# Optimization experiments

Measured on AMD Instinct MI355X. Metric: run time of the kernel, lower is better.

Reference implementation:

```python
import jax, jax.numpy as jnp
import numpy as np

N = 32768      # tokens
E = 2048       # embedding_dim
V = 256        # vq_dim
K = 256        # codebook size (levels=[256] -> single level, log2 K = 8)
HID = 1024     # condition MLP hidden dim
LOG2K = 8      # log2_num_embeddings
N_MID = 4      # condition_layer - 2 middle blocks
BN_EPS = 1e-5


def _normalize(x):
    return x / (jnp.linalg.norm(x, axis=-1, keepdims=True) + 1e-6)


def _bn(x, g, b):
    # BatchNorm1d, training-mode batch statistics over the codebook rows
    m = x.mean(0)
    v = x.var(0)
    return g * (x - m) * jax.lax.rsqrt(v + BN_EPS) + b


def _codebook(w0, b0, g0, be0, wm, bm, gm, bem, wL, bL):
    # get_bvectors(8, 256): binary expansion of 0..255, width 8 (no pad needed)
    ints = jnp.arange(K)
    bits = ((ints[:, None] >> jnp.arange(LOG2K - 1, -1, -1)[None, :]) & 1).astype(jnp.float32)
    x = jax.nn.relu(_bn(bits @ w0 + b0, g0, be0))
    for i in range(N_MID):
        x = jax.nn.relu(_bn(x @ wm[i] + bm[i], gm[i], bem[i]))
    return x @ wL + bL  # [K, V]


def setup_inputs() -> dict:
    key = jax.random.key(0)
    ks = jax.random.split(key, 8)
    def lin(k, fan_in, shape):
        return (jax.random.normal(k, shape, jnp.float32) / np.sqrt(fan_in)).astype(jnp.float32)
    return {
        "h_in": jax.random.normal(ks[0], (N, E), jnp.float32),
        "temp": jnp.array([0.3], jnp.float32),
        "proj_w": lin(ks[1], E, (E, V)), "proj_b": jnp.zeros((V,), jnp.float32),
        "pinv_w": lin(ks[2], V, (V, E)), "pinv_b": jnp.zeros((E,), jnp.float32),
        "w0": lin(ks[3], LOG2K, (LOG2K, HID)), "b0": jnp.zeros((HID,), jnp.float32),
        "g0": jnp.ones((HID,), jnp.float32), "be0": jnp.zeros((HID,), jnp.float32),
        "wm": lin(ks[4], HID, (N_MID, HID, HID)), "bm": jnp.zeros((N_MID, HID), jnp.float32),
        "gm": jnp.ones((N_MID, HID), jnp.float32), "bem": jnp.zeros((N_MID, HID), jnp.float32),
        "wL": lin(ks[5], HID, (HID, V)), "bL": jnp.zeros((V,), jnp.float32),
    }


def reference(h_in, temp, proj_w, proj_b, pinv_w, pinv_b,
              w0, b0, g0, be0, wm, bm, gm, bem, wL, bL):
    # forward(h_in, mode='eval', temperature=1, level=256); levels=[256] -> idx_all=1
    h = _normalize(h_in @ proj_w + proj_b)                          # proj + sphere normalize, [N, V]
    embed = _normalize(_codebook(w0, b0, g0, be0, wm, bm, gm, bem, wL, bL))  # [K, V]

    # attention(): distance logits with temperature-scaled detached term
    sim = h @ embed.T                                               # [N, K]
    alpha = 1.0 / temp ** 2
    distances = -2.0 * (alpha - 1.0) * jax.lax.stop_gradient(sim) - 2.0 * sim
    A = jax.nn.softmax(-distances, axis=1)                          # [N, K]

    k_code, k_p = jax.random.split(jax.random.key(42))
    code = jax.random.categorical(k_code, -distances, axis=-1)      # multinomial(A, 1), [N]
    onehot = jax.nn.one_hot(code, K, dtype=A.dtype)
    c = onehot * (1.0 - A) + (1.0 - onehot) * (-A)
    A2 = A + jax.lax.stop_gradient(c)                               # fwd value == onehot
    h_vq = h + A2 @ embed - jax.lax.stop_gradient(h)                # straight-through quantize
    vq_loss = jnp.linalg.norm(h_vq - h, axis=-1).mean()             # idx_all == 1

    # select = (0 < p) & (p < 1) since idx=0, idx_all=1
    p = jax.random.uniform(k_p, (h.shape[0],))
    select = (0.0 < p) & (p < 1.0)
    quantized = h_vq * select[:, None].astype(h_vq.dtype)
    probs = A * select[:, None].astype(A.dtype)
    vq_code = code * select.astype(code.dtype)

    quantized_inv = quantized @ pinv_w + pinv_b                     # [N, E]
    return quantized_inv, vq_code, quantized, probs, vq_loss
```

## Files before the change

### kernel.cpp

```cpp
#include <hip/hip_runtime.h>
#include <hip/hip_bf16.h>
#include <stdint.h>
#include <stddef.h>

#ifndef PARTITIONABLE
#define PARTITIONABLE 1
#endif

typedef __attribute__((ext_vector_type(8))) short short8;
typedef __attribute__((ext_vector_type(4))) short short4v;
typedef __attribute__((ext_vector_type(4))) float f32x4;

__host__ __device__ __forceinline__ uint32_t rotl32(uint32_t x, int d){ return (x<<d)|(x>>(32-d)); }

__host__ __device__ __forceinline__ void tf4(uint32_t&x0, uint32_t&x1, int r0,int r1,int r2,int r3){
  x0+=x1; x1=rotl32(x1,r0); x1^=x0;
  x0+=x1; x1=rotl32(x1,r1); x1^=x0;
  x0+=x1; x1=rotl32(x1,r2); x1^=x0;
  x0+=x1; x1=rotl32(x1,r3); x1^=x0;
}
__host__ __device__ __forceinline__ void threefry2x32(uint32_t k0,uint32_t k1,uint32_t x0,uint32_t x1,
                                                      uint32_t&y0,uint32_t&y1){
  uint32_t ks2 = k0^k1^0x1BD11BDAu;
  x0+=k0; x1+=k1;
  tf4(x0,x1,13,15,26,6);  x0+=k1;  x1+=ks2+1u;
  tf4(x0,x1,17,29,16,24); x0+=ks2; x1+=k0+2u;
  tf4(x0,x1,13,15,26,6);  x0+=k0;  x1+=k1+3u;
  tf4(x0,x1,17,29,16,24); x0+=k1;  x1+=ks2+4u;
  tf4(x0,x1,13,15,26,6);  x0+=ks2; x1+=k0+5u;
  y0=x0; y1=x1;
}

__device__ __forceinline__ uint32_t random_bits32(uint32_t k0,uint32_t k1,uint32_t idx, uint32_t half){
#if PARTITIONABLE
  uint32_t y0,y1; threefry2x32(k0,k1, 0u, idx, y0,y1);
  (void)half;
  return y0 ^ y1;
#else
  uint32_t y0,y1;
  if (idx < half) { threefry2x32(k0,k1, idx, idx+half, y0,y1); return y0; }
  else            { threefry2x32(k0,k1, idx-half, idx, y0,y1); return y1; }
#endif
}

__device__ __forceinline__ unsigned short bf16_rne(float x){
  unsigned u = __float_as_uint(x);
  unsigned r = (u + 0x7FFFu + ((u>>16)&1u)) >> 16;
  return (unsigned short)r;
}
__device__ __forceinline__ float bf16_tof(unsigned short h){
  return __uint_as_float(((unsigned)h)<<16);
}
__device__ __forceinline__ void split8(const float* src, short8& hi, short8& lo){
  #pragma unroll
  for (int e=0;e<8;e++){
    unsigned short h = bf16_rne(src[e]);
    hi[e] = (short)h;
    lo[e] = (short)bf16_rne(src[e] - bf16_tof(h));
  }
}
__device__ __forceinline__ void split4(const float* src, short4v& hi, short4v& lo){
  #pragma unroll
  for (int e=0;e<4;e++){
    unsigned short h = bf16_rne(src[e]);
    hi[e] = (short)h;
    lo[e] = (short)bf16_rne(src[e] - bf16_tof(h));
  }
}

__device__ __forceinline__ void gll16(const void* g, void* l){
  __builtin_amdgcn_global_load_lds(
      (const __attribute__((address_space(1))) unsigned int*)g,
      (__attribute__((address_space(3))) unsigned int*)l, 16, 0, 0);
}

__device__ __forceinline__ void mk1_gemm(const float* __restrict__ A, int lda,
                                         const unsigned short* __restrict__ packB,
                                         int K, char* smem, f32x4 (&acc)[2][4]){
  const int tid=threadIdx.x, lane=tid&63, wv=tid>>6;
  const int wr=wv>>2, wc=wv&3;
  const int arow=tid>>3, aseg=tid&7, swA=(arow>>1)&3;
  unsigned short* Ahi=(unsigned short*)smem;
  unsigned short* Alo=(unsigned short*)(smem+4096);
  unsigned short* Bhi=(unsigned short*)(smem+8192);
  unsigned short* Blo=(unsigned short*)(smem+24576);
  const int NT=K/32;
  const int sA = arow*32 + ((aseg>>1)^swA)*8 + (aseg&1)*4;
  const int seg = wv*2;

  float4 av = *(const float4*)(A + (size_t)arow*lda + aseg*4);
  for(int t=0;t<NT;t++){
    __syncthreads();
    {
      float af[4]={av.x,av.y,av.z,av.w}; short4v vh,vl; split4(af,vh,vl);
      *(short4v*)&Ahi[sA]=vh; *(short4v*)&Alo[sA]=vl;
      const unsigned short* src = packB + (size_t)t*16384;
      #pragma unroll
      for(int q=0;q<2;q++){
        gll16(src + (seg+q)*512 + lane*8,        (char*)Bhi + (seg+q)*1024);
        gll16(src + 8192 + (seg+q)*512 + lane*8, (char*)Blo + (seg+q)*1024);
      }
      if (t+1<NT) av = *(const float4*)(A + (size_t)arow*lda + (t+1)*32 + aseg*4);
    }
    __syncthreads();
    short8 ah[2],al[2],bh[4],bl[4];
    const int kg=lane>>4;
    #pragma unroll
    for(int i=0;i<2;i++){
      const int r = wr*32 + i*16 + (lane&15);
      const int offA = r*32 + ((kg ^ ((r>>1)&3))*8);
      ah[i]=*(const short8*)&Ahi[offA]; al[i]=*(const short8*)&Alo[offA];
    }
    #pragma unroll
    for(int j=0;j<4;j++){
      const int c = wc*64 + j*16 + (lane&15);
      const int offB = c*32 + ((kg ^ ((c>>1)&3))*8);
      bh[j]=*(const short8*)&Bhi[offB]; bl[j]=*(const short8*)&Blo[offB];
    }
    #pragma unroll
    for(int i=0;i<2;i++)
      #pragma unroll
      for(int j=0;j<4;j++){
        acc[i][j]=__builtin_amdgcn_mfma_f32_16x16x32_bf16(ah[i],bh[j],acc[i][j],0,0,0);
        acc[i][j]=__builtin_amdgcn_mfma_f32_16x16x32_bf16(ah[i],bl[j],acc[i][j],0,0,0);
        acc[i][j]=__builtin_amdgcn_mfma_f32_16x16x32_bf16(al[i],bh[j],acc[i][j],0,0,0);
      }
  }
}

__global__ __launch_bounds__(256) void pack_w_kernel(const float* __restrict__ W,
                                                     unsigned short* __restrict__ pack){
  const int t = blockIdx.x>>2, s = blockIdx.x&3, c = threadIdx.x;
  const int g = s ^ ((c>>1)&3);
  const float* p = W + (size_t)(t*32 + g*8)*256 + c;
  float bf[8];
  #pragma unroll
  for(int e=0;e<8;e++) bf[e]=p[(size_t)e*256];
  short8 h,l; split8(bf,h,l);
  unsigned short* dst = pack + (size_t)t*16384 + c*32 + s*8;
  *(short8*)dst = h;
  *(short8*)(dst+8192) = l;
}

__device__ __forceinline__ void bn_block_t(float (&acc)[4], int col0,
                                           const float* __restrict__ gma,
                                           const float* __restrict__ bta,
                                           float* __restrict__ Yt,
                                           float* Zs, float* red, float* mcol, float* vcol){
  const int r = threadIdx.x;
  #pragma unroll
  for (int j=0;j<4;j++) Zs[r*5+j] = acc[j];
  __syncthreads();
  if (r < 16){
    const int rl = r & 3, j = r >> 2;
    float s = 0.f;
    for (int rr=rl; rr<256; rr+=4) s += Zs[rr*5+j];
    red[rl*4+j] = s;
  }
  __syncthreads();
  if (r < 4)
    mcol[r] = (red[0*4+r]+red[1*4+r]+red[2*4+r]+red[3*4+r]) * (1.0f/256.0f);
  __syncthreads();
  if (r < 16){
    const int rl = r & 3, j = r >> 2;
    const float m = mcol[j];
    float s2 = 0.f;
    for (int rr=rl; rr<256; rr+=4){ float d = Zs[rr*5+j]-m; s2 += d*d; }
    red[rl*4+j] = s2;
  }
  __syncthreads();
  if (r < 4)
    vcol[r] = (red[0*4+r]+red[1*4+r]+red[2*4+r]+red[3*4+r]) * (1.0f/256.0f);
  __syncthreads();
  #pragma unroll
  for (int j=0;j<4;j++){
    const int c = col0 + j;
    const float scale = gma[c] * rsqrtf(vcol[j] + 1e-5f);
    const float sh = bta[c];
    const float v = (acc[j]-mcol[j])*scale + sh;
    Yt[(size_t)c*256 + r] = v > 0.f ? v : 0.f;
  }
}

__global__ __launch_bounds__(256) void mlp_layer2_kernel(
    const float* __restrict__ Xt, const float* __restrict__ W,
    const float* __restrict__ bias,
    const float* __restrict__ gma, const float* __restrict__ bta,
    float* __restrict__ Yt){
  __shared__ float Ws[1024*2];
  __shared__ float Zs[256*3];
  __shared__ float red[8], mcol[2], vcol[2];
  const int r = threadIdx.x;
  const int col0 = blockIdx.x*2;
  #pragma unroll
  for (int q=0;q<4;q++){
    const int k = q*256 + r;
    const float2 wv = *(const float2*)&W[(size_t)k*1024 + col0];
    *(float2*)&Ws[k*2] = wv;
  }
  __syncthreads();
  float acc0=0.f, acc1=0.f;
  #pragma unroll 16
  for (int k=0;k<1024;k++){
    const float a = Xt[(size_t)k*256 + r];
    acc0 += a*Ws[k*2];
    acc1 += a*Ws[k*2+1];
  }
  acc0 += bias[col0]; acc1 += bias[col0+1];
  Zs[r*3+0]=acc0; Zs[r*3+1]=acc1;
  __syncthreads();
  if (r < 8){
    const int rl = r & 3, j = r >> 2;
    float s=0.f;
    for (int rr=rl; rr<256; rr+=4) s += Zs[rr*3+j];
    red[rl*2+j] = s;
  }
  __syncthreads();
  if (r < 2) mcol[r] = (red[0*2+r]+red[1*2+r]+red[2*2+r]+red[3*2+r])*(1.0f/256.0f);
  __syncthreads();
  if (r < 8){
    const int rl = r & 3, j = r >> 2;
    const float m = mcol[j];
    float s2=0.f;
    for (int rr=rl; rr<256; rr+=4){ float d = Zs[rr*3+j]-m; s2 += d*d; }
    red[rl*2+j] = s2;
  }
  __syncthreads();
  if (r < 2) vcol[r] = (red[0*2+r]+red[1*2+r]+red[2*2+r]+red[3*2+r])*(1.0f/256.0f);
  __syncthreads();
  {
    const float s0 = gma[col0] * rsqrtf(vcol[0] + 1e-5f);
    const float v0 = (acc0-mcol[0])*s0 + bta[col0];
    Yt[(size_t)col0*256 + r] = v0 > 0.f ? v0 : 0.f;
    const float s1 = gma[col0+1] * rsqrtf(vcol[1] + 1e-5f);
    const float v1 = (acc1-mcol[1])*s1 + bta[col0+1];
    Yt[(size_t)(col0+1)*256 + r] = v1 > 0.f ? v1 : 0.f;
  }
}

__global__ __launch_bounds__(256) void mlp_l0t_kernel(
    const float* __restrict__ w0, const float* __restrict__ b0,
    const float* __restrict__ g0, const float* __restrict__ be0,
    float* __restrict__ Yt){
  __shared__ float Zs[256*5];
  __shared__ float red[16], mcol[4], vcol[4];
  const int i = threadIdx.x;
  const int col0 = blockIdx.x*4;
  float acc[4];
  #pragma unroll
  for (int j=0;j<4;j++) acc[j] = b0[col0+j];
  #pragma unroll
  for (int jj=0;jj<8;jj++){
    if ((i >> (7-jj)) & 1){
      #pragma unroll
      for (int j=0;j<4;j++) acc[j] += w0[jj*1024 + col0 + j];
    }
  }
  bn_block_t(acc, col0, g0, be0, Yt, Zs, red, mcol, vcol);
}

__global__ __launch_bounds__(256) void mlp_tail_kernel(
    const float* __restrict__ Xt,
    const float* __restrict__ wL, const float* __restrict__ bL,
    const float* __restrict__ pinv_w, const float* __restrict__ pinv_b,
    float* __restrict__ embed, unsigned short* __restrict__ packE,
    float* __restrict__ Epp){
  __shared__ float xrow[1024];
  __shared__ float erow[256];
  __shared__ float wsum[4];
  const int n = blockIdx.x, t = threadIdx.x;
  #pragma unroll
  for (int q=0;q<4;q++) xrow[q*256+t] = Xt[(size_t)(q*256+t)*256 + n];
  __syncthreads();
  float acc = 0.f;
  #pragma unroll 16
  for (int k=0;k<1024;k++) acc += xrow[k] * wL[(size_t)k*256 + t];
  acc += bL[t];
  const int lane = t & 63, wv = t >> 6;
  float v = acc*acc;
  #pragma unroll
  for (int o=32;o;o>>=1) v += __shfl_xor(v,o);
  if (lane==0) wsum[wv]=v;
  __syncthreads();
  const float total = wsum[0]+wsum[1]+wsum[2]+wsum[3];
  const float inv = 1.0f/(sqrtf(total)+1e-6f);
  const float y = acc*inv;
  embed[(size_t)n*256+t] = y;
  erow[t] = y;
  {
    unsigned short h = bf16_rne(y);
    unsigned short l = bf16_rne(y - bf16_tof(h));
    const int tt=t>>5, kk=t&31, g=kk>>3, e=kk&7, s=g^((n>>1)&3);
    unsigned short* d = packE + (size_t)tt*16384 + n*32 + s*8 + e;
    d[0] = h; d[8192] = l;
  }
  __syncthreads();
  float a8[8] = {0.f,0.f,0.f,0.f,0.f,0.f,0.f,0.f};
  #pragma unroll 8
  for (int k=0;k<256;k++){
    const float ev = erow[k];
    const float4 w0v = *(const float4*)&pinv_w[(size_t)k*2048 + t*8];
    const float4 w1v = *(const float4*)&pinv_w[(size_t)k*2048 + t*8 + 4];
    a8[0] += ev*w0v.x; a8[1] += ev*w0v.y; a8[2] += ev*w0v.z; a8[3] += ev*w0v.w;
    a8[4] += ev*w1v.x; a8[5] += ev*w1v.y; a8[6] += ev*w1v.z; a8[7] += ev*w1v.w;
  }
  #pragma unroll
  for (int j=0;j<8;j++) a8[j] += pinv_b[t*8+j];
  float4* dst = (float4*)(Epp + (size_t)n*2048 + t*8);
  dst[0] = (float4){a8[0],a8[1],a8[2],a8[3]};
  dst[1] = (float4){a8[4],a8[5],a8[6],a8[7]};
}

__global__ __launch_bounds__(512) void proj_norm_kernel(
    const float* __restrict__ A, const unsigned short* __restrict__ packW,
    const float* __restrict__ bias, float* __restrict__ Hn, int K){
  __shared__ char smem[40960];
  f32x4 acc[2][4];
  #pragma unroll
  for (int i=0;i<2;i++)
    #pragma unroll
    for (int j=0;j<4;j++) acc[i][j] = (f32x4){0.f,0.f,0.f,0.f};
  const int bm = blockIdx.x * 64;
  mk1_gemm(A + (size_t)bm*K, K, packW, K, smem, acc);
  __syncthreads();

  const int tid = threadIdx.x, lane = tid&63, wv = tid>>6;
  const int wr = wv>>2, wc = wv&3;
  float* ns = (float*)smem;
  #pragma unroll
  for (int j=0;j<4;j++){
    const int c = wc*64 + j*16 + (lane&15);
    const float bb = bias[c];
    #pragma unroll
    for (int i=0;i<2;i++)
      #pragma unroll
      for (int reg=0;reg<4;reg++) acc[i][j][reg] += bb;
  }
  #pragma unroll
  for (int i=0;i<2;i++)
    #pragma unroll
    for (int reg=0;reg<4;reg++){
      float p = acc[i][0][reg]*acc[i][0][reg] + acc[i][1][reg]*acc[i][1][reg]
              + acc[i][2][reg]*acc[i][2][reg] + acc[i][3][reg]*acc[i][3][reg];
      #pragma unroll
      for (int o=1;o<16;o<<=1) p += __shfl_xor(p, o);
      if ((lane&15)==0) ns[wc*64 + wr*32 + i*16 + (lane>>4)*4 + reg] = p;
    }
  __syncthreads();
  #pragma unroll
  for (int i=0;i<2;i++){
    const int rl = wr*32 + i*16 + (lane>>4)*4;
    #pragma unroll
    for (int reg=0;reg<4;reg++){
      const int r = rl + reg;
      const float tot = ns[0*64+r]+ns[1*64+r]+ns[2*64+r]+ns[3*64+r];
      const float inv = 1.0f/(sqrtf(tot)+1e-6f);
      const size_t grow = (size_t)(bm + r);
      #pragma unroll
      for (int j=0;j<4;j++){
        const int c = wc*64 + j*16 + (lane&15);
        Hn[grow*256 + c] = acc[i][j][reg]*inv;
      }
    }
  }
}

__global__ __launch_bounds__(512) void sim_sample_kernel(
    const float* __restrict__ Hn, const unsigned short* __restrict__ packE,
    const float* __restrict__ embed, const float* __restrict__ temp,
    float* __restrict__ probs, float* __restrict__ codef,
    float* __restrict__ quant, float* __restrict__ norms,
    const float* __restrict__ Epp, const float* __restrict__ pinv_b,
    float* __restrict__ q_inv,
    uint32_t kc0, uint32_t kc1, uint32_t kp0, uint32_t kp1){
  __shared__ char smem[40960];
  f32x4 acc[2][4];
  #pragma unroll
  for (int i=0;i<2;i++)
    #pragma unroll
    for (int j=0;j<4;j++) acc[i][j] = (f32x4){0.f,0.f,0.f,0.f};
  const int bm = blockIdx.x * 64;
  mk1_gemm(Hn + (size_t)bm*256, 256, packE, 256, smem, acc);
  __syncthreads();

  float* redf = (float*)smem;
  int*   redi = (int*)(smem+1024);
  float* smax = (float*)(smem+2048);
  float* ssum = (float*)(smem+2304);
  float* ssel = (float*)(smem+2560);
  int*  scode = (int*)(smem+2816);

  const int tid = threadIdx.x, lane = tid&63, wv = tid>>6;
  const int wr = wv>>2, wc = wv&3;
  const float tv = temp[0];
  const float alpha = 1.0f/(tv*tv);
  #pragma unroll
  for (int i=0;i<2;i++)
    #pragma unroll
    for (int j=0;j<4;j++)
      #pragma unroll
      for (int reg=0;reg<4;reg++){
        const float s = acc[i][j][reg];
        const float dist = -2.0f*(alpha-1.0f)*s - 2.0f*s;
        acc[i][j][reg] = -dist;
      }
  #pragma unroll
  for (int i=0;i<2;i++)
    #pragma unroll
    for (int reg=0;reg<4;reg++){
      float m = fmaxf(fmaxf(acc[i][0][reg], acc[i][1][reg]),
                      fmaxf(acc[i][2][reg], acc[i][3][reg]));
      #pragma unroll
      for (int o=1;o<16;o<<=1) m = fmaxf(m, __shfl_xor(m, o));
      if ((lane&15)==0) redf[wc*64 + wr*32 + i*16 + (lane>>4)*4 + reg] = m;
    }
  __syncthreads();
  if (tid < 64)
    smax[tid] = fmaxf(fmaxf(redf[0*64+tid], redf[1*64+tid]), fmaxf(redf[2*64+tid], redf[3*64+tid]));
  __syncthreads();
  #pragma unroll
  for (int i=0;i<2;i++)
    #pragma unroll
    for (int reg=0;reg<4;reg++){
      const int r = wr*32 + i*16 + (lane>>4)*4 + reg;
      const float m = smax[r];
      float p = expf(acc[i][0][reg]-m) + expf(acc[i][1][reg]-m)
              + expf(acc[i][2][reg]-m) + expf(acc[i][3][reg]-m);
      #pragma unroll
      for (int o=1;o<16;o<<=1) p += __shfl_xor(p, o);
      if ((lane&15)==0) redf[wc*64 + r] = p;
    }
  __syncthreads();
  if (tid < 64){
    ssum[tid] = redf[0*64+tid]+redf[1*64+tid]+redf[2*64+tid]+redf[3*64+tid];
    const uint32_t pb = random_bits32(kp0,kp1,(uint32_t)(bm+tid), 16384u);
    const float pf = __uint_as_float((pb>>9) | 0x3f800000u) - 1.0f;
    ssel[tid] = (pf > 0.0f) ? 1.0f : 0.0f;
  }
  __syncthreads();
  #pragma unroll
  for (int i=0;i<2;i++)
    #pragma unroll
    for (int reg=0;reg<4;reg++){
      const int r = wr*32 + i*16 + (lane>>4)*4 + reg;
      const uint32_t grow = (uint32_t)(bm + r);
      float zb = -1e38f; int ib = 0x7fffffff;
      #pragma unroll
      for (int j=0;j<4;j++){
        const int c = wc*64 + j*16 + (lane&15);
        const uint32_t bits = random_bits32(kc0,kc1, grow*256u + (uint32_t)c, 4194304u);
        const float f = __uint_as_float((bits>>9) | 0x3f800000u) - 1.0f;
        const float TINY = 1.17549435082228751e-38f;
        const float u = fmaxf(TINY, f + TINY);
        const float g = -logf(-logf(u));
        const float z = acc[i][j][reg] + g;
        if (z > zb || (z == zb && c < ib)){ zb = z; ib = c; }
      }
      #pragma unroll
      for (int o=1;o<16;o<<=1){
        const float zo = __shfl_xor(zb, o); const int io = __shfl_xor(ib, o);
        if (zo > zb || (zo == zb && io < ib)){ zb = zo; ib = io; }
      }
      if ((lane&15)==0){ redf[wc*64 + r] = zb; redi[wc*64 + r] = ib; }
    }
  __syncthreads();
  if (tid < 64){
    float zb = redf[0*64+tid]; int ib = redi[0*64+tid];
    #pragma unroll
    for (int w=1; w<4; w++)
      if (redf[w*64+tid] > zb || (redf[w*64+tid] == zb && redi[w*64+tid] < ib)){
        zb = redf[w*64+tid]; ib = redi[w*64+tid];
      }
    scode[tid] = ib;
  }
  __syncthreads();
  #pragma unroll
  for (int i=0;i<2;i++)
    #pragma unroll
    for (int reg=0;reg<4;reg++){
      const int r = wr*32 + i*16 + (lane>>4)*4 + reg;
      const size_t grow = (size_t)(bm + r);
      const float m = smax[r], sum = ssum[r], sel = ssel[r];
      const int code = scode[r];
      float p2 = 0.f;
      #pragma unroll
      for (int j=0;j<4;j++){
        const int c = wc*64 + j*16 + (lane&15);
        const float e = expf(acc[i][j][reg] - m);
        probs[grow*256 + c] = (e/sum) * sel;
        const float ev = embed[(size_t)code*256 + c];
        quant[grow*256 + c] = ev * sel;
        const float d = ev - Hn[grow*256 + c];
        p2 += d*d;
      }
      #pragma unroll
      for (int o=1;o<16;o<<=1) p2 += __shfl_xor(p2, o);
      if ((lane&15)==0) redf[wc*64 + r] = p2;
    }
  __syncthreads();
  if (tid < 64){
    norms[bm+tid] = sqrtf(redf[0*64+tid]+redf[1*64+tid]+redf[2*64+tid]+redf[3*64+tid]);
    codef[bm+tid] = (float)scode[tid] * ssel[tid];
  }
  #pragma unroll
  for (int rr=0; rr<8; rr++){
    const int r = wv*8 + rr;
    const int code = scode[r];
    const float sel = ssel[r];
    const float4* s4 = (const float4*)((sel != 0.0f) ? (Epp + (size_t)code*2048) : pinv_b);
    float4* dst = (float4*)(q_inv + (size_t)(bm + r)*2048);
    #pragma unroll
    for (int q=0;q<8;q++) dst[q*64 + lane] = s4[q*64 + lane];
  }
}

__global__ __launch_bounds__(256) void loss_kernel(const float* __restrict__ norms,
                                                   float* __restrict__ outp){
  const int t = threadIdx.x;
  float s = 0.f;
  for (int i=t;i<32768;i+=256) s += norms[i];
  #pragma unroll
  for (int o=32;o;o>>=1) s += __shfl_xor(s,o);
  __shared__ float wred[4];
  if ((t&63)==0) wred[t>>6]=s;
  __syncthreads();
  if (t==0) outp[0] = (wred[0]+wred[1]+wred[2]+wred[3]) * (1.0f/32768.0f);
}

extern "C" void kernel_launch(void* const* d_in, const int* in_sizes, int n_in,
                              void* d_out, int out_size, void* d_ws, size_t ws_size,
                              hipStream_t stream){
  const float* h_in  = (const float*)d_in[0];
  const float* temp  = (const float*)d_in[1];
  const float* proj_w= (const float*)d_in[2];
  const float* proj_b= (const float*)d_in[3];
  const float* pinv_w= (const float*)d_in[4];
  const float* pinv_b= (const float*)d_in[5];
  const float* w0 = (const float*)d_in[6];
  const float* b0 = (const float*)d_in[7];
  const float* g0 = (const float*)d_in[8];
  const float* be0= (const float*)d_in[9];
  const float* wm = (const float*)d_in[10];
  const float* bm = (const float*)d_in[11];
  const float* gm = (const float*)d_in[12];
  const float* bem= (const float*)d_in[13];
  const float* wL = (const float*)d_in[14];
  const float* bL = (const float*)d_in[15];

  float* out = (float*)d_out;
  float* q_inv  = out;
  float* o_code = out + 67108864;
  float* o_quant= out + 67141632;
  float* o_probs= out + 75530240;
  float* o_loss = out + 83918848;

  float* ws = (float*)d_ws;
  float* Hn     = ws + 0;
  float* XtA    = ws + 8388608;
  float* XtB    = ws + 8650752;
  float* embed  = ws + 8912896;
  float* norms  = ws + 8978432;
  float* Epp    = ws + 9076736;
  unsigned short* packW = (unsigned short*)(ws + 9601024);
  unsigned short* packE = (unsigned short*)(ws + 10125312);

  uint32_t kc0,kc1,kp0,kp1;
#if PARTITIONABLE
  threefry2x32(0u,42u, 0u,0u, kc0,kc1);
  threefry2x32(0u,42u, 0u,1u, kp0,kp1);
#else
  { uint32_t a0,b0w,a1,b1w;
    threefry2x32(0u,42u, 0u,2u, a0,b0w);
    threefry2x32(0u,42u, 1u,3u, a1,b1w);
    kc0=a0; kc1=a1; kp0=b0w; kp1=b1w; }
#endif

  pack_w_kernel<<<256,256,0,stream>>>(proj_w, packW);

  proj_norm_kernel<<<512,512,0,stream>>>(h_in, packW, proj_b, Hn, 2048);

  mlp_l0t_kernel<<<256,256,0,stream>>>(w0, b0, g0, be0, XtA);
  mlp_layer2_kernel<<<512,256,0,stream>>>(XtA, wm + 0*1048576, bm + 0*1024, gm + 0*1024, bem + 0*1024, XtB);
  mlp_layer2_kernel<<<512,256,0,stream>>>(XtB, wm + 1*1048576, bm + 1*1024, gm + 1*1024, bem + 1*1024, XtA);
  mlp_layer2_kernel<<<512,256,0,stream>>>(XtA, wm + 2*1048576, bm + 2*1024, gm + 2*1024, bem + 2*1024, XtB);
  mlp_layer2_kernel<<<512,256,0,stream>>>(XtB, wm + 3*1048576, bm + 3*1024, gm + 3*1024, bem + 3*1024, XtA);
  mlp_tail_kernel<<<256,256,0,stream>>>(XtA, wL, bL, pinv_w, pinv_b, embed, packE, Epp);

  sim_sample_kernel<<<512,512,0,stream>>>(Hn, packE, embed, temp,
                                          o_probs, o_code, o_quant, norms,
                                          Epp, pinv_b, q_inv,
                                          kc0,kc1,kp0,kp1);
  loss_kernel<<<1,256,0,stream>>>(norms, o_loss);
}
```

Baseline: 521.5 us.

## Fuse codebook MLP chain into one persistent kernel with grid barriers

Replaces the weight-pack kernel and the six separate codebook MLP kernels (first layer, four middle layers, tail) with one 256-block persistent kernel. The layers are separated by a software grid barrier built on atomic flags that are reset by a memset. Each block now handles four columns per middle layer instead of two, so only half as many blocks are needed. The aim is to remove launch overhead and inter-kernel gaps on the small serial MLP chain. The risks are deadlock if the 256 blocks are not all co-resident, and barrier spin cost.

```diff
diff --git a/kernel.cpp b/kernel.cpp
--- a/kernel.cpp
+++ b/kernel.cpp
@@ -128,18 +128,24 @@
   }
 }
 
-__global__ __launch_bounds__(256) void pack_w_kernel(const float* __restrict__ W,
-                                                     unsigned short* __restrict__ pack){
-  const int t = blockIdx.x>>2, s = blockIdx.x&3, c = threadIdx.x;
-  const int g = s ^ ((c>>1)&3);
-  const float* p = W + (size_t)(t*32 + g*8)*256 + c;
-  float bf[8];
-  #pragma unroll
-  for(int e=0;e<8;e++) bf[e]=p[(size_t)e*256];
-  short8 h,l; split8(bf,h,l);
-  unsigned short* dst = pack + (size_t)t*16384 + c*32 + s*8;
-  *(short8*)dst = h;
-  *(short8*)(dst+8192) = l;
+__device__ __forceinline__ void xbar(uint32_t gen, uint32_t* flags, uint32_t* release){
+  __syncthreads();
+  if (threadIdx.x == 0){
+    __threadfence();
+    __hip_atomic_store(&flags[blockIdx.x], gen, __ATOMIC_RELAXED, __HIP_MEMORY_SCOPE_AGENT);
+  }
+  if (blockIdx.x == 0){
+    while (__hip_atomic_load(&flags[threadIdx.x], __ATOMIC_RELAXED, __HIP_MEMORY_SCOPE_AGENT) < gen)
+      __builtin_amdgcn_s_sleep(16);
+    __syncthreads();
+    if (threadIdx.x == 0)
+      __hip_atomic_store(release, gen, __ATOMIC_RELAXED, __HIP_MEMORY_SCOPE_AGENT);
+  } else if (threadIdx.x == 0){
+    while (__hip_atomic_load(release, __ATOMIC_RELAXED, __HIP_MEMORY_SCOPE_AGENT) < gen)
+      __builtin_amdgcn_s_sleep(16);
+  }
+  __syncthreads();
+  __threadfence();
 }
 
 __device__ __forceinline__ void bn_block_t(float (&acc)[4], int col0,
@@ -182,31 +188,9 @@
   }
 }
 
-__global__ __launch_bounds__(256) void mlp_layer2_kernel(
-    const float* __restrict__ Xt, const float* __restrict__ W,
-    const float* __restrict__ bias,
-    const float* __restrict__ gma, const float* __restrict__ bta,
-    float* __restrict__ Yt){
-  __shared__ float Ws[1024*2];
-  __shared__ float Zs[256*3];
-  __shared__ float red[8], mcol[2], vcol[2];
-  const int r = threadIdx.x;
-  const int col0 = blockIdx.x*2;
-  #pragma unroll
-  for (int q=0;q<4;q++){
-    const int k = q*256 + r;
-    const float2 wv = *(const float2*)&W[(size_t)k*1024 + col0];
-    *(float2*)&Ws[k*2] = wv;
-  }
-  __syncthreads();
-  float acc0=0.f, acc1=0.f;
-  #pragma unroll 16
-  for (int k=0;k<1024;k++){
-    const float a = Xt[(size_t)k*256 + r];
-    acc0 += a*Ws[k*2];
-    acc1 += a*Ws[k*2+1];
-  }
-  acc0 += bias[col0]; acc1 += bias[col0+1];
+__device__ __forceinline__ void bn2(float acc0, float acc1, int col0,
+    const float* __restrict__ gma, const float* __restrict__ bta, float* __restrict__ Yt,
+    float* Zs, float* red, float* mcol, float* vcol, int r){
   Zs[r*3+0]=acc0; Zs[r*3+1]=acc1;
   __syncthreads();
   if (r < 8){
@@ -228,87 +212,146 @@
   __syncthreads();
   if (r < 2) vcol[r] = (red[0*2+r]+red[1*2+r]+red[2*2+r]+red[3*2+r])*(1.0f/256.0f);
   __syncthreads();
-  {
-    const float s0 = gma[col0] * rsqrtf(vcol[0] + 1e-5f);
-    const float v0 = (acc0-mcol[0])*s0 + bta[col0];
-    Yt[(size_t)col0*256 + r] = v0 > 0.f ? v0 : 0.f;
-    const float s1 = gma[col0+1] * rsqrtf(vcol[1] + 1e-5f);
-    const float v1 = (acc1-mcol[1])*s1 + bta[col0+1];
-    Yt[(size_t)(col0+1)*256 + r] = v1 > 0.f ? v1 : 0.f;
-  }
-}
-
-__global__ __launch_bounds__(256) void mlp_l0t_kernel(
+  const float s0 = gma[col0] * rsqrtf(vcol[0] + 1e-5f);
+  const float v0 = (acc0-mcol[0])*s0 + bta[col0];
+  Yt[(size_t)col0*256 + r] = v0 > 0.f ? v0 : 0.f;
+  const float s1 = gma[col0+1] * rsqrtf(vcol[1] + 1e-5f);
+  const float v1 = (acc1-mcol[1])*s1 + bta[col0+1];
+  Yt[(size_t)(col0+1)*256 + r] = v1 > 0.f ? v1 : 0.f;
+}
+
+__device__ void mid_layer(int b, int r, char* um,
+    const float* __restrict__ Xt, const float* __restrict__ W,
+    const float* __restrict__ bias,
+    const float* __restrict__ gma, const float* __restrict__ bta,
+    float* __restrict__ Yt){
+  float* Ws  = (float*)um;
+  float* Zs  = (float*)(um+16384);
+  float* red = (float*)(um+19456);
+  float* mcol= (float*)(um+19488);
+  float* vcol= (float*)(um+19496);
+  const int cA = b*2, cB = b*2 + 512;
+  #pragma unroll
+  for (int q=0;q<4;q++){
+    const int k = q*256 + r;
+    const float2 wa = *(const float2*)&W[(size_t)k*1024 + cA];
+    const float2 wb = *(const float2*)&W[(size_t)k*1024 + cB];
+    *(float4*)&Ws[k*4] = (float4){wa.x, wa.y, wb.x, wb.y};
+  }
+  __syncthreads();
+  float a0=0.f,a1=0.f,a2=0.f,a3=0.f;
+  #pragma unroll 16
+  for (int k=0;k<1024;k++){
+    const float a = Xt[(size_t)k*256 + r];
+    const float4 wv = *(const float4*)&Ws[k*4];
+    a0 += a*wv.x; a1 += a*wv.y; a2 += a*wv.z; a3 += a*wv.w;
+  }
+  a0 += bias[cA]; a1 += bias[cA+1]; a2 += bias[cB]; a3 += bias[cB+1];
+  bn2(a0, a1, cA, gma, bta, Yt, Zs, red, mcol, vcol, r);
+  __syncthreads();
+  bn2(a2, a3, cB, gma, bta, Yt, Zs, red, mcol, vcol, r);
+}
+
+__global__ __launch_bounds__(256) void uber_mlp_kernel(
+    const float* __restrict__ proj_w, unsigned short* __restrict__ packW,
     const float* __restrict__ w0, const float* __restrict__ b0,
     const float* __restrict__ g0, const float* __restrict__ be0,
-    float* __restrict__ Yt){
-  __shared__ float Zs[256*5];
-  __shared__ float red[16], mcol[4], vcol[4];
-  const int i = threadIdx.x;
-  const int col0 = blockIdx.x*4;
-  float acc[4];
-  #pragma unroll
-  for (int j=0;j<4;j++) acc[j] = b0[col0+j];
-  #pragma unroll
-  for (int jj=0;jj<8;jj++){
-    if ((i >> (7-jj)) & 1){
-      #pragma unroll
-      for (int j=0;j<4;j++) acc[j] += w0[jj*1024 + col0 + j];
-    }
-  }
-  bn_block_t(acc, col0, g0, be0, Yt, Zs, red, mcol, vcol);
-}
-
-__global__ __launch_bounds__(256) void mlp_tail_kernel(
-    const float* __restrict__ Xt,
+    const float* __restrict__ wm, const float* __restrict__ bm_a,
+    const float* __restrict__ gm, const float* __restrict__ bem,
     const float* __restrict__ wL, const float* __restrict__ bL,
     const float* __restrict__ pinv_w, const float* __restrict__ pinv_b,
+    float* __restrict__ XtA, float* __restrict__ XtB,
     float* __restrict__ embed, unsigned short* __restrict__ packE,
-    float* __restrict__ Epp){
-  __shared__ float xrow[1024];
-  __shared__ float erow[256];
-  __shared__ float wsum[4];
-  const int n = blockIdx.x, t = threadIdx.x;
-  #pragma unroll
-  for (int q=0;q<4;q++) xrow[q*256+t] = Xt[(size_t)(q*256+t)*256 + n];
-  __syncthreads();
-  float acc = 0.f;
-  #pragma unroll 16
-  for (int k=0;k<1024;k++) acc += xrow[k] * wL[(size_t)k*256 + t];
-  acc += bL[t];
-  const int lane = t & 63, wv = t >> 6;
-  float v = acc*acc;
-  #pragma unroll
-  for (int o=32;o;o>>=1) v += __shfl_xor(v,o);
-  if (lane==0) wsum[wv]=v;
-  __syncthreads();
-  const float total = wsum[0]+wsum[1]+wsum[2]+wsum[3];
-  const float inv = 1.0f/(sqrtf(total)+1e-6f);
-  const float y = acc*inv;
-  embed[(size_t)n*256+t] = y;
-  erow[t] = y;
+    float* __restrict__ Epp,
+    uint32_t* __restrict__ flags, uint32_t* __restrict__ release){
+  __shared__ char um[20608];
+  const int b = blockIdx.x, tid = threadIdx.x;
+
   {
-    unsigned short h = bf16_rne(y);
-    unsigned short l = bf16_rne(y - bf16_tof(h));
-    const int tt=t>>5, kk=t&31, g=kk>>3, e=kk&7, s=g^((n>>1)&3);
-    unsigned short* d = packE + (size_t)tt*16384 + n*32 + s*8 + e;
-    d[0] = h; d[8192] = l;
-  }
-  __syncthreads();
-  float a8[8] = {0.f,0.f,0.f,0.f,0.f,0.f,0.f,0.f};
-  #pragma unroll 8
-  for (int k=0;k<256;k++){
-    const float ev = erow[k];
-    const float4 w0v = *(const float4*)&pinv_w[(size_t)k*2048 + t*8];
-    const float4 w1v = *(const float4*)&pinv_w[(size_t)k*2048 + t*8 + 4];
-    a8[0] += ev*w0v.x; a8[1] += ev*w0v.y; a8[2] += ev*w0v.z; a8[3] += ev*w0v.w;
-    a8[4] += ev*w1v.x; a8[5] += ev*w1v.y; a8[6] += ev*w1v.z; a8[7] += ev*w1v.w;
-  }
-  #pragma unroll
-  for (int j=0;j<8;j++) a8[j] += pinv_b[t*8+j];
-  float4* dst = (float4*)(Epp + (size_t)n*2048 + t*8);
-  dst[0] = (float4){a8[0],a8[1],a8[2],a8[3]};
-  dst[1] = (float4){a8[4],a8[5],a8[6],a8[7]};
+    const int t = b>>2, s = b&3, c = tid;
+    const int g = s ^ ((c>>1)&3);
+    const float* p = proj_w + (size_t)(t*32 + g*8)*256 + c;
+    float bf[8];
+    #pragma unroll
+    for(int e=0;e<8;e++) bf[e]=p[(size_t)e*256];
+    short8 h,l; split8(bf,h,l);
+    unsigned short* dst = packW + (size_t)t*16384 + c*32 + s*8;
+    *(short8*)dst = h;
+    *(short8*)(dst+8192) = l;
+  }
+  {
+    float* Zs  = (float*)um;
+    float* red = (float*)(um+5120);
+    float* mcol= (float*)(um+5184);
+    float* vcol= (float*)(um+5200);
+    const int col0 = b*4;
+    float acc[4];
+    #pragma unroll
+    for (int j=0;j<4;j++) acc[j] = b0[col0+j];
+    #pragma unroll
+    for (int jj=0;jj<8;jj++){
+      if ((tid >> (7-jj)) & 1){
+        #pragma unroll
+        for (int j=0;j<4;j++) acc[j] += w0[jj*1024 + col0 + j];
+      }
+    }
+    bn_block_t(acc, col0, g0, be0, XtA, Zs, red, mcol, vcol);
+  }
+  xbar(1, flags, release);
+  mid_layer(b, tid, um, XtA, wm + 0*1048576, bm_a + 0*1024, gm + 0*1024, bem + 0*1024, XtB);
+  xbar(2, flags, release);
+  mid_layer(b, tid, um, XtB, wm + 1*1048576, bm_a + 1*1024, gm + 1*1024, bem + 1*1024, XtA);
+  xbar(3, flags, release);
+  mid_layer(b, tid, um, XtA, wm + 2*1048576, bm_a + 2*1024, gm + 2*1024, bem + 2*1024, XtB);
+  xbar(4, flags, release);
+  mid_layer(b, tid, um, XtB, wm + 3*1048576, bm_a + 3*1024, gm + 3*1024, bem + 3*1024, XtA);
+  xbar(5, flags, release);
+  {
+    float* xrow = (float*)um;
+    float* erow = (float*)(um+4096);
+    float* wsum = (float*)(um+5120);
+    const int n = b, t = tid;
+    #pragma unroll
+    for (int q=0;q<4;q++) xrow[q*256+t] = XtA[(size_t)(q*256+t)*256 + n];
+    __syncthreads();
+    float acc = 0.f;
+    #pragma unroll 16
+    for (int k=0;k<1024;k++) acc += xrow[k] * wL[(size_t)k*256 + t];
+    acc += bL[t];
+    const int lane = t & 63, wv = t >> 6;
+    float v = acc*acc;
+    #pragma unroll
+    for (int o=32;o;o>>=1) v += __shfl_xor(v,o);
+    if (lane==0) wsum[wv]=v;
+    __syncthreads();
+    const float total = wsum[0]+wsum[1]+wsum[2]+wsum[3];
+    const float inv = 1.0f/(sqrtf(total)+1e-6f);
+    const float y = acc*inv;
+    embed[(size_t)n*256+t] = y;
+    erow[t] = y;
+    {
+      unsigned short h = bf16_rne(y);
+      unsigned short l = bf16_rne(y - bf16_tof(h));
+      const int tt=t>>5, kk=t&31, g=kk>>3, e=kk&7, s=g^((n>>1)&3);
+      unsigned short* d = packE + (size_t)tt*16384 + n*32 + s*8 + e;
+      d[0] = h; d[8192] = l;
+    }
+    __syncthreads();
+    float a8[8] = {0.f,0.f,0.f,0.f,0.f,0.f,0.f,0.f};
+    #pragma unroll 8
+    for (int k=0;k<256;k++){
+      const float ev = erow[k];
+      const float4 w0v = *(const float4*)&pinv_w[(size_t)k*2048 + t*8];
+      const float4 w1v = *(const float4*)&pinv_w[(size_t)k*2048 + t*8 + 4];
+      a8[0] += ev*w0v.x; a8[1] += ev*w0v.y; a8[2] += ev*w0v.z; a8[3] += ev*w0v.w;
+      a8[4] += ev*w1v.x; a8[5] += ev*w1v.y; a8[6] += ev*w1v.z; a8[7] += ev*w1v.w;
+    }
+    #pragma unroll
+    for (int j=0;j<8;j++) a8[j] += pinv_b[t*8+j];
+    float4* dst = (float4*)(Epp + (size_t)n*2048 + t*8);
+    dst[0] = (float4){a8[0],a8[1],a8[2],a8[3]};
+    dst[1] = (float4){a8[4],a8[5],a8[6],a8[7]};
+  }
 }
 
 __global__ __launch_bounds__(512) void proj_norm_kernel(
@@ -563,6 +606,8 @@
   float* Epp    = ws + 9076736;
   unsigned short* packW = (unsigned short*)(ws + 9601024);
   unsigned short* packE = (unsigned short*)(ws + 10125312);
+  uint32_t* flags   = (uint32_t*)(ws + 11000000);
+  uint32_t* release = (uint32_t*)(ws + 11000256);
 
   uint32_t kc0,kc1,kp0,kp1;
 #if PARTITIONABLE
@@ -575,16 +620,15 @@
     kc0=a0; kc1=a1; kp0=b0w; kp1=b1w; }
 #endif
 
-  pack_w_kernel<<<256,256,0,stream>>>(proj_w, packW);
+  hipMemsetAsync(flags, 0, (256+1)*sizeof(uint32_t), stream);
+
+  uber_mlp_kernel<<<256,256,0,stream>>>(proj_w, packW,
+                                        w0,b0,g0,be0, wm,bm,gm,bem, wL,bL,
+                                        pinv_w,pinv_b,
+                                        XtA,XtB, embed,packE,Epp,
+                                        flags, release);
 
   proj_norm_kernel<<<512,512,0,stream>>>(h_in, packW, proj_b, Hn, 2048);
-
-  mlp_l0t_kernel<<<256,256,0,stream>>>(w0, b0, g0, be0, XtA);
-  mlp_layer2_kernel<<<512,256,0,stream>>>(XtA, wm + 0*1048576, bm + 0*1024, gm + 0*1024, bem + 0*1024, XtB);
-  mlp_layer2_kernel<<<512,256,0,stream>>>(XtB, wm + 1*1048576, bm + 1*1024, gm + 1*1024, bem + 1*1024, XtA);
-  mlp_layer2_kernel<<<512,256,0,stream>>>(XtA, wm + 2*1048576, bm + 2*1024, gm + 2*1024, bem + 2*1024, XtB);
-  mlp_layer2_kernel<<<512,256,0,stream>>>(XtB, wm + 3*1048576, bm + 3*1024, gm + 3*1024, bem + 3*1024, XtA);
-  mlp_tail_kernel<<<256,256,0,stream>>>(XtA, wL, bL, pinv_w, pinv_b, embed, packE, Epp);
 
   sim_sample_kernel<<<512,512,0,stream>>>(Hn, packE, embed, temp,
                                           o_probs, o_code, o_quant, norms,
```

New measurement: 641.9 us. 1.23x slower.
